# Optimization experiments

Measured on AMD Instinct MI355X. Metric: run time of the kernel, lower is better.

The kernel has to match this reference:

```python
import jax, jax.numpy as jnp
import numpy as np

A = 1.0  # slope of hard sigmoid (init arg `a`)


def setup_inputs() -> dict:
    key = jax.random.key(0)
    ks = jax.random.split(key, 10)
    H, B, BOT, TOP = 1024, 4096, 1024, 1024
    stdv = 1.0 / np.sqrt(H)
    u = lambda k, shp: jax.random.uniform(k, shp, jnp.float32, -stdv, stdv)
    U_11 = u(ks[0], (4 * H + 1, H))
    U_21 = u(ks[1], (4 * H + 1, TOP))
    W_01 = u(ks[2], (4 * H + 1, BOT))
    bias = u(ks[3], (4 * H + 1,))
    c = jax.random.normal(ks[4], (H, B), jnp.float32) * 0.1
    h = jnp.tanh(jax.random.normal(ks[5], (H, B), jnp.float32))
    h_bottom = jnp.tanh(jax.random.normal(ks[6], (BOT, B), jnp.float32))
    h_top = jnp.tanh(jax.random.normal(ks[7], (TOP, B), jnp.float32))
    z = (jax.random.uniform(ks[8], (1, B)) > 0.5).astype(jnp.float32)
    z_bottom = (jax.random.uniform(ks[9], (1, B)) > 0.5).astype(jnp.float32)
    return dict(c=c, h_bottom=h_bottom, h=h, h_top=h_top, z=z,
                z_bottom=z_bottom, U_11=U_11, U_21=U_21, W_01=W_01, bias=bias)


def reference(c, h_bottom, h, h_top, z, z_bottom, U_11, U_21, W_01, bias):
    H = U_11.shape[1]
    # [4H+1, B] pre-activations: recurrent + gated top-down + gated bottom-up + bias
    f_s = (W_01 @ h_bottom
           + z * (U_21 @ h_top)
           + z_bottom * (U_11 @ h)
           + bias[:, None])
    f = jax.nn.sigmoid(f_s[0:H])
    i = jax.nn.sigmoid(f_s[H:2 * H])
    o = jax.nn.sigmoid(f_s[2 * H:3 * H])
    g = jnp.tanh(f_s[3 * H:4 * H])
    z_hat = jnp.clip((f_s[4 * H:4 * H + 1] * A + 1.0) / 2.0, 0.0, 1.0)  # hard_sigm
    one = 1.0
    c_new = (z * (i * g)
             + (one - z) * (one - z_bottom) * c
             + (one - z) * z_bottom * (f * c + i * g))
    tanh_c = jnp.tanh(c_new)
    h_new = (z * o * tanh_c
             + (one - z) * (one - z_bottom) * h
             + (one - z) * z_bottom * o * tanh_c)
    # straight-through binary boundary: forward step(z_hat>0.5), backward identity
    z_new = z_hat + jax.lax.stop_gradient((z_hat > 0.5).astype(z_hat.dtype) - z_hat)
    return h_new, c_new, z_new
```

## Files before the change

### kernel.cpp

```cpp
#include <hip/hip_runtime.h>
#include <hip/hip_bf16.h>
#include <math.h>

#define Hd   1024
#define Bsz  4096
#define Kc   3072
#define NT   48

typedef unsigned short u16;
typedef __attribute__((ext_vector_type(8))) u16 u16x8;
typedef __attribute__((ext_vector_type(2))) u16 u16x2;
typedef __attribute__((ext_vector_type(4))) float f32x4;
typedef __attribute__((ext_vector_type(8))) short bf16x8;

template<bool V> struct BoolC { static constexpr bool value = V; };

__device__ inline u16 f2bf(float f) {
    __hip_bfloat16 h = __float2bfloat16(f);
    return *reinterpret_cast<u16*>(&h);
}

__device__ inline float sigm(float x) { return 1.0f / (1.0f + __expf(-x)); }

__device__ inline void gload16(const void* g, const void* s) {
    __builtin_amdgcn_global_load_lds(
        (const __attribute__((address_space(1))) void*)g,
        (__attribute__((address_space(3))) void*)s, 16, 0, 0);
}

#define BAR()   __builtin_amdgcn_s_barrier()
#define VMW(n)  asm volatile("s_waitcnt vmcnt(" #n ")" ::: "memory")

__global__ __launch_bounds__(256) void prep_A(const float* __restrict__ U11,
                                              const float* __restrict__ U21,
                                              const float* __restrict__ W01,
                                              u16* __restrict__ Ab,
                                              float* __restrict__ out) {
    if (blockIdx.x == 0) {
        float* outz = out + (size_t)2 * Hd * Bsz;
        for (int i = threadIdx.x; i < Bsz; i += 256) outz[i] = 0.0f;
    }
    int t = blockIdx.x * 256 + threadIdx.x;
    int row = t / 384;
    int kc = (t - row * 384) * 8;
    int r = row >> 2, gate = row & 3;
    int sel = kc >> 10;
    int k = kc & 1023;
    const float* src = (sel == 0) ? W01 : ((sel == 1) ? U21 : U11);
    const float4* p = reinterpret_cast<const float4*>(src + (size_t)(gate * Hd + r) * Hd + k);
    float4 v0 = p[0], v1 = p[1];
    u16x8 o;
    o[0] = f2bf(v0.x); o[1] = f2bf(v0.y); o[2] = f2bf(v0.z); o[3] = f2bf(v0.w);
    o[4] = f2bf(v1.x); o[5] = f2bf(v1.y); o[6] = f2bf(v1.z); o[7] = f2bf(v1.w);
    *reinterpret_cast<u16x8*>(Ab + (size_t)row * Kc + kc) = o;
}

__global__ __launch_bounds__(256) void prep_B(const float* __restrict__ hb,
                                              const float* __restrict__ ht,
                                              const float* __restrict__ hh,
                                              const float* __restrict__ z,
                                              const float* __restrict__ zb,
                                              const float* __restrict__ U11,
                                              const float* __restrict__ U21,
                                              const float* __restrict__ W01,
                                              u16* __restrict__ Bb,
                                              float* __restrict__ out) {
    __shared__ float tile[64][33];
    __shared__ float red[8][32];
    int n0 = blockIdx.x * 32;
    int kg0 = blockIdx.y * 64;
    int sel = kg0 >> 10;
    int k0 = kg0 & 1023;
    const float* src = (sel == 0) ? hb : ((sel == 1) ? ht : hh);
    const float* wsrc = (sel == 0) ? W01 : ((sel == 1) ? U21 : U11);
    int t = threadIdx.x, tx = t & 31, ty = t >> 5;
#pragma unroll
    for (int j = 0; j < 8; ++j) {
        int kk = ty * 8 + j;
        tile[kk][tx] = src[(size_t)(k0 + kk) * Bsz + n0 + tx];
    }
    __syncthreads();
    {
        int kp = t & 31, ny = t >> 5;
#pragma unroll
        for (int j = 0; j < 4; ++j) {
            int nl = ny * 4 + j;
            int n = n0 + nl;
            float s = (sel == 0) ? 1.0f : ((sel == 1) ? z[n] : zb[n]);
            u16x2 o;
            o[0] = f2bf(tile[kp * 2][nl] * s);
            o[1] = f2bf(tile[kp * 2 + 1][nl] * s);
            *reinterpret_cast<u16x2*>(Bb + (size_t)n * Kc + kg0 + kp * 2) = o;
        }
    }
    {
        int col = t & 31, seg = t >> 5;
        const float* w = wsrc + (size_t)4096 * 1024 + k0 + seg * 8;
        float p = 0.0f;
#pragma unroll
        for (int j = 0; j < 8; ++j) p += w[j] * tile[seg * 8 + j][col];
        red[seg][col] = p;
        __syncthreads();
        if (seg == 0) {
            float tot = 0.0f;
#pragma unroll
            for (int q = 0; q < 8; ++q) tot += red[q][col];
            int n = n0 + col;
            float sca = (sel == 0) ? 1.0f : ((sel == 1) ? z[n] : zb[n]);
            atomicAdd(out + (size_t)2 * Hd * Bsz + n, tot * sca);
        }
    }
}

__global__ __launch_bounds__(512, 2) void gemm_fused(
    const u16* __restrict__ A, const u16* __restrict__ Bm,
    const float* __restrict__ c_in, const float* __restrict__ h_in,
    const float* __restrict__ z, const float* __restrict__ zb,
    const float* __restrict__ bias, float* __restrict__ out) {
    extern __shared__ __align__(16) u16 smem[];
    u16* const AsB = smem;
    u16* const BsB = smem + 32768;

    const int t = threadIdx.x;
    const int w = t >> 6, l = t & 63;
    const int wm = w >> 2, wn = w & 3;

    const int orig = blockIdx.x;
    const int wg = ((orig & 7) << 5) | (orig >> 3);
    const int bm = wg >> 4, bn = wg & 15;

    const int srow = t >> 3;
    const int sgs  = (t & 7) ^ (srow & 7);
    const int fr = l & 15, fq = l >> 4, fkey = l & 7;

    f32x4 acc[8][4];
#pragma unroll
    for (int i = 0; i < 8; ++i)
#pragma unroll
        for (int j = 0; j < 4; ++j) acc[i][j] = (f32x4){0.f, 0.f, 0.f, 0.f};

    const u16* gA = A  + (size_t)(bm * 256 + srow) * Kc + sgs * 8;
    const u16* gB = Bm + (size_t)(bn * 256 + srow) * Kc + sgs * 8;

    auto stageA = [&](int buf, int half, int kt) {
#pragma unroll
        for (int iss = 0; iss < 2; ++iss) {
            const u16* g = gA + (size_t)(half * 128 + iss * 64) * Kc + kt * 64;
            const u16* d = AsB + buf * 16384 + (half * 128 + iss * 64 + (w << 3)) * 64;
            gload16(g, d);
        }
    };
    auto stageB = [&](int buf, int half, int kt) {
#pragma unroll
        for (int iss = 0; iss < 2; ++iss) {
            const u16* g = gB + (size_t)(half * 128 + iss * 64) * Kc + kt * 64;
            const u16* d = BsB + buf * 16384 + (half * 128 + iss * 64 + (w << 3)) * 64;
            gload16(g, d);
        }
    };

    bf16x8 aF[2][4][2];
    bf16x8 bF[2][2][2];

    auto readA = [&](int buf, int mh, int miL, int ks) -> bf16x8 {
        int r = mh * 128 + wm * 64 + miL * 16 + fr;
        int g = ((ks << 2) + fq) ^ fkey;
        return *reinterpret_cast<const bf16x8*>(AsB + buf * 16384 + r * 64 + g * 8);
    };
    auto readB = [&](int buf, int nh, int niL, int ks) -> bf16x8 {
        int r = nh * 128 + wn * 32 + niL * 16 + fr;
        int g = ((ks << 2) + fq) ^ fkey;
        return *reinterpret_cast<const bf16x8*>(BsB + buf * 16384 + r * 64 + g * 8);
    };

    stageA(0, 0, 0); stageB(0, 0, 0); stageA(0, 1, 0); stageB(0, 1, 0);

    auto ktile = [&](int tc, auto pfc) {
        constexpr bool pf = decltype(pfc)::value;
        const int cur = tc & 1, nxt = cur ^ 1;
        if constexpr (pf) { VMW(4); stageA(nxt, 0, tc + 1); stageB(nxt, 0, tc + 1); }
        else             { VMW(4); }
        BAR();
#pragma unroll
        for (int mi = 0; mi < 4; ++mi) {
            aF[0][mi][0] = readA(cur, 0, mi, 0); aF[0][mi][1] = readA(cur, 0, mi, 1);
        }
#pragma unroll
        for (int ni = 0; ni < 2; ++ni) {
            bF[0][ni][0] = readB(cur, 0, ni, 0); bF[0][ni][1] = readB(cur, 0, ni, 1);
        }
        BAR();
        __builtin_amdgcn_s_setprio(1);
#pragma unroll
        for (int mi = 0; mi < 4; ++mi)
#pragma unroll
            for (int ni = 0; ni < 2; ++ni)
#pragma unroll
                for (int ks = 0; ks < 2; ++ks)
                    acc[mi][ni] = __builtin_amdgcn_mfma_f32_16x16x32_bf16(
                        aF[0][mi][ks], bF[0][ni][ks], acc[mi][ni], 0, 0, 0);
        __builtin_amdgcn_s_setprio(0);
        if constexpr (pf) { VMW(6); stageA(nxt, 1, tc + 1); stageB(nxt, 1, tc + 1); }
        else             { VMW(2); }
        BAR();
#pragma unroll
        for (int mi = 0; mi < 4; ++mi) {
            aF[1][mi][0] = readA(cur, 1, mi, 0); aF[1][mi][1] = readA(cur, 1, mi, 1);
        }
        BAR();
        __builtin_amdgcn_s_setprio(1);
#pragma unroll
        for (int mi = 0; mi < 4; ++mi)
#pragma unroll
            for (int ni = 0; ni < 2; ++ni)
#pragma unroll
                for (int ks = 0; ks < 2; ++ks)
                    acc[4 + mi][ni] = __builtin_amdgcn_mfma_f32_16x16x32_bf16(
                        aF[1][mi][ks], bF[0][ni][ks], acc[4 + mi][ni], 0, 0, 0);
        __builtin_amdgcn_s_setprio(0);
        if constexpr (pf) { VMW(8); } else { VMW(0); }
        BAR();
#pragma unroll
        for (int ni = 0; ni < 2; ++ni) {
            bF[1][ni][0] = readB(cur, 1, ni, 0); bF[1][ni][1] = readB(cur, 1, ni, 1);
        }
        BAR();
        __builtin_amdgcn_s_setprio(1);
#pragma unroll
        for (int mi = 0; mi < 4; ++mi)
#pragma unroll
            for (int ni = 0; ni < 2; ++ni)
#pragma unroll
                for (int ks = 0; ks < 2; ++ks)
                    acc[4 + mi][2 + ni] = __builtin_amdgcn_mfma_f32_16x16x32_bf16(
                        aF[1][mi][ks], bF[1][ni][ks], acc[4 + mi][2 + ni], 0, 0, 0);
        __builtin_amdgcn_s_setprio(0);
        __builtin_amdgcn_s_setprio(1);
#pragma unroll
        for (int mi = 0; mi < 4; ++mi)
#pragma unroll
            for (int ni = 0; ni < 2; ++ni)
#pragma unroll
                for (int ks = 0; ks < 2; ++ks)
                    acc[mi][2 + ni] = __builtin_amdgcn_mfma_f32_16x16x32_bf16(
                        aF[0][mi][ks], bF[1][ni][ks], acc[mi][2 + ni], 0, 0, 0);
        __builtin_amdgcn_s_setprio(0);
    };

    for (int tc = 0; tc < NT - 1; ++tc) ktile(tc, BoolC<true>{});
    ktile(NT - 1, BoolC<false>{});

    const int rB = bm * 64;
    const int nB = bn * 256;
    float zc[4], zbv[4];
#pragma unroll
    for (int ni = 0; ni < 4; ++ni) {
        int n = nB + (ni >> 1) * 128 + wn * 32 + (ni & 1) * 16 + fr;
        zc[ni] = z[n]; zbv[ni] = zb[n];
    }
#pragma unroll
    for (int mi = 0; mi < 8; ++mi) {
        const int r = rB + (mi >> 2) * 32 + wm * 16 + (mi & 3) * 4 + fq;
        const float b0 = bias[r], b1 = bias[Hd + r], b2 = bias[2 * Hd + r], b3 = bias[3 * Hd + r];
        const float* crow = c_in + (size_t)r * Bsz;
        const float* hrow = h_in + (size_t)r * Bsz;
        float* hout = out + (size_t)r * Bsz;
        float* cout = out + (size_t)Hd * Bsz + (size_t)r * Bsz;
#pragma unroll
        for (int ni = 0; ni < 4; ++ni) {
            const int n = nB + (ni >> 1) * 128 + wn * 32 + (ni & 1) * 16 + fr;
            f32x4 a = acc[mi][ni];
            float co = crow[n], ho = hrow[n];
            float fg = sigm(a[0] + b0);
            float ig = sigm(a[1] + b1);
            float og = sigm(a[2] + b2);
            float gg = tanhf(a[3] + b3);
            float i_g = ig * gg;
            float nz = 1.0f - zc[ni], nzb = 1.0f - zbv[ni];
            float cn = zc[ni] * i_g + nz * nzb * co + nz * zbv[ni] * (fg * co + i_g);
            float tc2 = tanhf(cn);
            float hn = zc[ni] * og * tc2 + nz * nzb * ho + nz * zbv[ni] * og * tc2;
            hout[n] = hn; cout[n] = cn;
        }
    }

    if (bm == 0 && t < 256) {
        float* outz = out + (size_t)2 * Hd * Bsz;
        int n = bn * 256 + t;
        float s = outz[n] + bias[4096];
        float zh = (s + 1.0f) * 0.5f;
        zh = fminf(fmaxf(zh, 0.0f), 1.0f);
        outz[n] = (zh > 0.5f) ? 1.0f : 0.0f;
    }
}

extern "C" void kernel_launch(void* const* d_in, const int* in_sizes, int n_in,
                              void* d_out, int out_size, void* d_ws, size_t ws_size,
                              hipStream_t stream) {
    (void)in_sizes; (void)n_in; (void)out_size; (void)ws_size;
    const float* c    = (const float*)d_in[0];
    const float* hb   = (const float*)d_in[1];
    const float* h    = (const float*)d_in[2];
    const float* ht   = (const float*)d_in[3];
    const float* z    = (const float*)d_in[4];
    const float* zb   = (const float*)d_in[5];
    const float* U11  = (const float*)d_in[6];
    const float* U21  = (const float*)d_in[7];
    const float* W01  = (const float*)d_in[8];
    const float* bias = (const float*)d_in[9];
    float* out = (float*)d_out;

    u16* Ab = (u16*)d_ws;
    u16* Bb = Ab + (size_t)4096 * Kc;

    hipFuncSetAttribute(reinterpret_cast<const void*>(gemm_fused),
                        hipFuncAttributeMaxDynamicSharedMemorySize, 131072);

    prep_A<<<6144, 256, 0, stream>>>(U11, U21, W01, Ab, out);
    prep_B<<<dim3(128, 48), 256, 0, stream>>>(hb, ht, h, z, zb, U11, U21, W01, Bb, out);
    gemm_fused<<<256, 512, 131072, stream>>>(Ab, Bb, c, h, z, zb, bias, out);
}
```

Measured before the change: 120.1 us.

## Restructure k-loop to interleave LDS reads, staged prefetch, and MFMA quadrants

Reorders the double-buffered GEMM k-tile loop so each LDS fragment read is followed by issuing one quarter of the next tile's global-to-LDS prefetch. Barriers now sit between MFMA quadrants, replacing the separate read/compute barrier pairs. This cuts the barriers per k-tile from six to four and spreads global loads across the tile to overlap them with MFMA work. The vmcnt wait counts were retuned, which risks a correctness hazard if a buffer is overwritten before all waves finish reading it.

```diff
diff --git a/kernel.cpp b/kernel.cpp
--- a/kernel.cpp
+++ b/kernel.cpp
@@ -30,6 +30,8 @@
 
 #define BAR()   __builtin_amdgcn_s_barrier()
 #define VMW(n)  asm volatile("s_waitcnt vmcnt(" #n ")" ::: "memory")
+#define PRIO1() __builtin_amdgcn_s_setprio(1)
+#define PRIO0() __builtin_amdgcn_s_setprio(0)
 
 __global__ __launch_bounds__(256) void prep_A(const float* __restrict__ U11,
                                               const float* __restrict__ U21,
@@ -173,82 +175,58 @@
         return *reinterpret_cast<const bf16x8*>(BsB + buf * 16384 + r * 64 + g * 8);
     };
 
+#define MFMAQ(mh, nh)                                                         \
+    PRIO1();                                                                  \
+    _Pragma("unroll")                                                         \
+    for (int mi = 0; mi < 4; ++mi)                                            \
+        _Pragma("unroll")                                                     \
+        for (int ni = 0; ni < 2; ++ni)                                        \
+            _Pragma("unroll")                                                 \
+            for (int ks = 0; ks < 2; ++ks)                                    \
+                acc[(mh)*4 + mi][(nh)*2 + ni] =                               \
+                    __builtin_amdgcn_mfma_f32_16x16x32_bf16(                  \
+                        aF[mh][mi][ks], bF[nh][ni][ks],                       \
+                        acc[(mh)*4 + mi][(nh)*2 + ni], 0, 0, 0);              \
+    PRIO0()
+
     stageA(0, 0, 0); stageB(0, 0, 0); stageA(0, 1, 0); stageB(0, 1, 0);
-
-    auto ktile = [&](int tc, auto pfc) {
-        constexpr bool pf = decltype(pfc)::value;
-        const int cur = tc & 1, nxt = cur ^ 1;
-        if constexpr (pf) { VMW(4); stageA(nxt, 0, tc + 1); stageB(nxt, 0, tc + 1); }
-        else             { VMW(4); }
+    VMW(4); BAR();
+
+    auto ktile = [&](int T, auto lastc) {
+        constexpr bool last = decltype(lastc)::value;
+        const int p = T & 1, q2 = p ^ 1;
+#pragma unroll
+        for (int j = 0; j < 4; ++j) {
+            aF[0][j][0] = readA(p, 0, j, 0); aF[0][j][1] = readA(p, 0, j, 1);
+        }
+#pragma unroll
+        for (int j = 0; j < 2; ++j) {
+            bF[0][j][0] = readB(p, 0, j, 0); bF[0][j][1] = readB(p, 0, j, 1);
+        }
+        if constexpr (!last) { stageA(q2, 0, T + 1); VMW(4); } else { VMW(2); }
         BAR();
-#pragma unroll
-        for (int mi = 0; mi < 4; ++mi) {
-            aF[0][mi][0] = readA(cur, 0, mi, 0); aF[0][mi][1] = readA(cur, 0, mi, 1);
-        }
-#pragma unroll
-        for (int ni = 0; ni < 2; ++ni) {
-            bF[0][ni][0] = readB(cur, 0, ni, 0); bF[0][ni][1] = readB(cur, 0, ni, 1);
-        }
+        MFMAQ(0, 0);
+#pragma unroll
+        for (int j = 0; j < 4; ++j) {
+            aF[1][j][0] = readA(p, 1, j, 0); aF[1][j][1] = readA(p, 1, j, 1);
+        }
+        if constexpr (!last) { stageB(q2, 0, T + 1); VMW(4); } else { VMW(0); }
         BAR();
-        __builtin_amdgcn_s_setprio(1);
-#pragma unroll
-        for (int mi = 0; mi < 4; ++mi)
-#pragma unroll
-            for (int ni = 0; ni < 2; ++ni)
-#pragma unroll
-                for (int ks = 0; ks < 2; ++ks)
-                    acc[mi][ni] = __builtin_amdgcn_mfma_f32_16x16x32_bf16(
-                        aF[0][mi][ks], bF[0][ni][ks], acc[mi][ni], 0, 0, 0);
-        __builtin_amdgcn_s_setprio(0);
-        if constexpr (pf) { VMW(6); stageA(nxt, 1, tc + 1); stageB(nxt, 1, tc + 1); }
-        else             { VMW(2); }
+        MFMAQ(1, 0);
+#pragma unroll
+        for (int j = 0; j < 2; ++j) {
+            bF[1][j][0] = readB(p, 1, j, 0); bF[1][j][1] = readB(p, 1, j, 1);
+        }
+        if constexpr (!last) stageA(q2, 1, T + 1);
         BAR();
-#pragma unroll
-        for (int mi = 0; mi < 4; ++mi) {
-            aF[1][mi][0] = readA(cur, 1, mi, 0); aF[1][mi][1] = readA(cur, 1, mi, 1);
-        }
+        MFMAQ(1, 1);
+        if constexpr (!last) { stageB(q2, 1, T + 1); VMW(4); }
         BAR();
-        __builtin_amdgcn_s_setprio(1);
-#pragma unroll
-        for (int mi = 0; mi < 4; ++mi)
-#pragma unroll
-            for (int ni = 0; ni < 2; ++ni)
-#pragma unroll
-                for (int ks = 0; ks < 2; ++ks)
-                    acc[4 + mi][ni] = __builtin_amdgcn_mfma_f32_16x16x32_bf16(
-                        aF[1][mi][ks], bF[0][ni][ks], acc[4 + mi][ni], 0, 0, 0);
-        __builtin_amdgcn_s_setprio(0);
-        if constexpr (pf) { VMW(8); } else { VMW(0); }
-        BAR();
-#pragma unroll
-        for (int ni = 0; ni < 2; ++ni) {
-            bF[1][ni][0] = readB(cur, 1, ni, 0); bF[1][ni][1] = readB(cur, 1, ni, 1);
-        }
-        BAR();
-        __builtin_amdgcn_s_setprio(1);
-#pragma unroll
-        for (int mi = 0; mi < 4; ++mi)
-#pragma unroll
-            for (int ni = 0; ni < 2; ++ni)
-#pragma unroll
-                for (int ks = 0; ks < 2; ++ks)
-                    acc[4 + mi][2 + ni] = __builtin_amdgcn_mfma_f32_16x16x32_bf16(
-                        aF[1][mi][ks], bF[1][ni][ks], acc[4 + mi][2 + ni], 0, 0, 0);
-        __builtin_amdgcn_s_setprio(0);
-        __builtin_amdgcn_s_setprio(1);
-#pragma unroll
-        for (int mi = 0; mi < 4; ++mi)
-#pragma unroll
-            for (int ni = 0; ni < 2; ++ni)
-#pragma unroll
-                for (int ks = 0; ks < 2; ++ks)
-                    acc[mi][2 + ni] = __builtin_amdgcn_mfma_f32_16x16x32_bf16(
-                        aF[0][mi][ks], bF[1][ni][ks], acc[mi][2 + ni], 0, 0, 0);
-        __builtin_amdgcn_s_setprio(0);
-    };
-
-    for (int tc = 0; tc < NT - 1; ++tc) ktile(tc, BoolC<true>{});
-    ktile(NT - 1, BoolC<false>{});
+        MFMAQ(0, 1);
+    };
+
+    for (int T = 0; T < NT - 1; ++T) ktile(T, BoolC<false>{});
+    ktile(NT - 1, BoolC<true>{});
 
     const int rB = bm * 64;
     const int nB = bn * 256;
@@ -292,6 +270,7 @@
         zh = fminf(fmaxf(zh, 0.0f), 1.0f);
         outz[n] = (zh > 0.5f) ? 1.0f : 0.0f;
     }
+#undef MFMAQ
 }
 
 extern "C" void kernel_launch(void* const* d_in, const int* in_sizes, int n_in,
```

Measured after the change: 115.7 us. 3.7% less time.
